# Optimization experiments

Measured on AMD Instinct MI355X. Metric: run time of the kernel, lower is better.

The kernel has to match this reference:

```python
import jax, jax.numpy as jnp
import numpy as np
import math

N_NODES = 50000
N_EDGES = 800000
HIDDEN = 128
NUM_GAUSS = 50
NUM_FILTERS = 128
CUTOFF = 10.0
SHIFT = math.log(2.0)


def setup_inputs() -> dict:
    key = jax.random.key(0)
    ks = jax.random.split(key, 12)
    x = jax.random.normal(ks[0], (N_NODES, HIDDEN), dtype=jnp.float32)
    edge_index = jax.random.randint(ks[1], (2, N_EDGES), 0, N_NODES, dtype=jnp.int64)
    edge_weight = jax.random.uniform(ks[2], (N_EDGES,), dtype=jnp.float32)
    edge_attr = jax.random.normal(ks[3], (N_EDGES, NUM_GAUSS), dtype=jnp.float32)
    # learned parameters (xavier-ish scale)
    def xavier(k, shape):
        fan_in, fan_out = shape[1], shape[0]
        bound = math.sqrt(6.0 / (fan_in + fan_out))
        return jax.random.uniform(k, shape, dtype=jnp.float32, minval=-bound, maxval=bound)
    mlp_w1 = xavier(ks[4], (NUM_FILTERS, NUM_GAUSS))
    mlp_b1 = jnp.zeros((NUM_FILTERS,), jnp.float32)
    mlp_w2 = xavier(ks[5], (NUM_FILTERS, NUM_FILTERS))
    mlp_b2 = jnp.zeros((NUM_FILTERS,), jnp.float32)
    lin1_w = xavier(ks[6], (NUM_FILTERS, HIDDEN))   # no bias
    lin2_w = xavier(ks[7], (HIDDEN, NUM_FILTERS))
    lin2_b = jnp.zeros((HIDDEN,), jnp.float32)
    lin_w = xavier(ks[8], (HIDDEN, HIDDEN))
    lin_b = jnp.zeros((HIDDEN,), jnp.float32)
    return {"x": x, "edge_index": edge_index, "edge_weight": edge_weight,
            "edge_attr": edge_attr, "mlp_w1": mlp_w1, "mlp_b1": mlp_b1,
            "mlp_w2": mlp_w2, "mlp_b2": mlp_b2, "lin1_w": lin1_w,
            "lin2_w": lin2_w, "lin2_b": lin2_b, "lin_w": lin_w, "lin_b": lin_b}


def shifted_softplus(v):
    return jax.nn.softplus(v) - SHIFT


def reference(x, edge_index, edge_weight, edge_attr, mlp_w1, mlp_b1,
              mlp_w2, mlp_b2, lin1_w, lin2_w, lin2_b, lin_w, lin_b):
    src, dst = edge_index[0], edge_index[1]
    # cosine cutoff per edge: [E]
    C = 0.5 * (jnp.cos(edge_weight * (jnp.pi / CUTOFF)) + 1.0)
    # edge filter MLP: [E, num_filters]
    h_e = shifted_softplus(edge_attr @ mlp_w1.T + mlp_b1)
    W = (h_e @ mlp_w2.T + mlp_b2) * C[:, None]
    # node projection, gather-multiply-scatter aggregation
    h = x @ lin1_w.T                       # [N, num_filters]
    msg = h[src] * W                       # [E, num_filters]
    agg = jax.ops.segment_sum(msg, dst, num_segments=N_NODES)  # [N, num_filters]
    h = agg @ lin2_w.T + lin2_b            # [N, hidden]
    h = shifted_softplus(h)
    out = h @ lin_w.T + lin_b              # [N, hidden]
    return out
```

## Files before the change

### kernel.cpp

```cpp
#include <hip/hip_runtime.h>
#include <hip/hip_bf16.h>
#include <math.h>

#define E_NUM 800000
#define NN 50000
#define NG 50
#define NTW (E_NUM / 16)
#define EDGE_BLOCKS 512

typedef __bf16 bf16x8 __attribute__((ext_vector_type(8)));
typedef float f32x4 __attribute__((ext_vector_type(4)));
typedef unsigned short ushortx8 __attribute__((ext_vector_type(8)));

__device__ __forceinline__ unsigned short f2b(float f) {
  union { __bf16 h; unsigned short u; } v; v.h = (__bf16)f; return v.u;
}
__device__ __forceinline__ float b2f(unsigned short u) {
  union { unsigned u; float f; } v; v.u = ((unsigned)u) << 16; return v.f;
}
__device__ __forceinline__ float sspf(float v) {
  float e = __builtin_amdgcn_exp2f(-1.4426950408889634f * fabsf(v));
  return fmaxf(v, 0.f) + 0.6931471805599453f * __builtin_amdgcn_logf(fmaf(0.5f, e, 0.5f));
}

__device__ __forceinline__ void gather_attr(const float* __restrict__ attr, int idx, int q,
                                            bf16x8& ua, bf16x8& ub) {
  const float* rp = attr + (long)idx * NG;
  float2 p0 = *(const float2*)(rp + q * 8);
  float2 p1 = *(const float2*)(rp + q * 8 + 2);
  float2 p2 = *(const float2*)(rp + q * 8 + 4);
  float2 p3 = *(const float2*)(rp + q * 8 + 6);
  float2 p4 = {0.f, 0.f}, p5 = {0.f, 0.f}, p6 = {0.f, 0.f}, p7 = {0.f, 0.f};
  if (q < 2) {
    const float* rp2 = rp + 32 + q * 8;
    p4 = *(const float2*)(rp2);
    p5 = *(const float2*)(rp2 + 2);
    p6 = *(const float2*)(rp2 + 4);
    p7 = *(const float2*)(rp2 + 6);
  } else if (q == 2) {
    p4 = *(const float2*)(rp + 48);
  }
  union { ushortx8 u; bf16x8 b; } a, bb;
  a.u[0] = f2b(p0.x); a.u[1] = f2b(p0.y); a.u[2] = f2b(p1.x); a.u[3] = f2b(p1.y);
  a.u[4] = f2b(p2.x); a.u[5] = f2b(p2.y); a.u[6] = f2b(p3.x); a.u[7] = f2b(p3.y);
  bb.u[0] = f2b(p4.x); bb.u[1] = f2b(p4.y); bb.u[2] = f2b(p5.x); bb.u[3] = f2b(p5.y);
  bb.u[4] = f2b(p6.x); bb.u[5] = f2b(p6.y); bb.u[6] = f2b(p7.x); bb.u[7] = f2b(p7.y);
  ua = a.b; ub = bb.b;
}

__global__ __launch_bounds__(256) void k_hist(const int* __restrict__ ei, int* __restrict__ counts) {
  int e = blockIdx.x * 256 + threadIdx.x;
  if (e < E_NUM) atomicAdd(&counts[ei[E_NUM + e]], 1);
}

__global__ __launch_bounds__(1024) void k_scan(const int* __restrict__ counts,
                                               int* __restrict__ cursor) {
  __shared__ int tot[1024];
  const int t = threadIdx.x;
  const int C = (NN + 1023) >> 10;
  int lo = t * C, hi = lo + C; if (hi > NN) hi = NN; if (lo > NN) lo = NN;
  int s = 0;
  for (int i = lo; i < hi; ++i) s += counts[i];
  tot[t] = s;
  __syncthreads();
  int mine = s;
  for (int o = 1; o < 1024; o <<= 1) {
    int v = (t >= o) ? tot[t - o] : 0;
    __syncthreads();
    tot[t] += v;
    __syncthreads();
  }
  int run = tot[t] - mine;
  for (int i = lo; i < hi; ++i) { int c = counts[i]; cursor[i] = run; run += c; }
}

__global__ __launch_bounds__(256) void k_scatter2(
    const int* __restrict__ ei, const float* __restrict__ ew,
    int* __restrict__ cursor, int* __restrict__ srcS, int* __restrict__ dstS,
    float* __restrict__ cS, int* __restrict__ eS)
{
  int e = blockIdx.x * 256 + threadIdx.x;
  if (e >= E_NUM) return;
  int d = ei[E_NUM + e];
  int pos = atomicAdd(&cursor[d], 1);
  srcS[pos] = ei[e];
  dstS[pos] = d;
  cS[pos] = 0.5f * (__builtin_amdgcn_cosf(ew[e] * 0.05f) + 1.f);
  eS[pos] = e;
}

__global__ __launch_bounds__(256) void k_mfma_gemm(
    const float* __restrict__ X, const float* __restrict__ Wm,
    const float* __restrict__ bias, float* __restrict__ out, int act, int nrows)
{
  __shared__ __attribute__((aligned(16))) unsigned short s_x[128 * 128];
  __shared__ __attribute__((aligned(16))) unsigned short s_w[128 * 128];
  const int tid = threadIdx.x;
  const int w = tid >> 6, lane = tid & 63, q = lane >> 4, n16 = lane & 15;
  const int base = blockIdx.x * 128;

  for (int c = tid; c < 128 * 16; c += 256) {
    int f = c >> 4, ch = c & 15;
    const float4* wp = (const float4*)(Wm + f * 128 + ch * 8);
    float4 v0 = wp[0], v1 = wp[1];
    ushortx8 v = { f2b(v0.x), f2b(v0.y), f2b(v0.z), f2b(v0.w),
                   f2b(v1.x), f2b(v1.y), f2b(v1.z), f2b(v1.w) };
    *(ushortx8*)&s_w[(f << 7) + ((ch ^ (f & 15)) << 3)] = v;
  }
  for (int c = tid; c < 128 * 16; c += 256) {
    int r = c >> 4, ch = c & 15;
    int n = base + r;
    float4 v0 = {0.f, 0.f, 0.f, 0.f}, v1 = v0;
    if (n < nrows) {
      const float4* xp = (const float4*)(X + (long)n * 128 + ch * 8);
      v0 = xp[0]; v1 = xp[1];
    }
    ushortx8 v = { f2b(v0.x), f2b(v0.y), f2b(v0.z), f2b(v0.w),
                   f2b(v1.x), f2b(v1.y), f2b(v1.z), f2b(v1.w) };
    *(ushortx8*)&s_x[(r << 7) + ((ch ^ (r & 15)) << 3)] = v;
  }
  __syncthreads();

  float bv[8];
#pragma unroll
  for (int t = 0; t < 8; ++t) bv[t] = bias ? bias[t * 16 + n16] : 0.f;

  bf16x8 a[2][4];
#pragma unroll
  for (int g = 0; g < 2; ++g) {
    int r = w * 32 + g * 16 + n16;
#pragma unroll
    for (int ks = 0; ks < 4; ++ks)
      a[g][ks] = *(const bf16x8*)&s_x[(r << 7) + (((ks * 4 + q) ^ (r & 15)) << 3)];
  }
#pragma unroll
  for (int t = 0; t < 8; ++t) {
    int f = t * 16 + n16;
    bf16x8 b[4];
#pragma unroll
    for (int ks = 0; ks < 4; ++ks)
      b[ks] = *(const bf16x8*)&s_w[(f << 7) + (((ks * 4 + q) ^ (f & 15)) << 3)];
#pragma unroll
    for (int g = 0; g < 2; ++g) {
      f32x4 acc = {0.f, 0.f, 0.f, 0.f};
#pragma unroll
      for (int ks = 0; ks < 4; ++ks)
        acc = __builtin_amdgcn_mfma_f32_16x16x32_bf16(a[g][ks], b[ks], acc, 0, 0, 0);
#pragma unroll
      for (int r = 0; r < 4; ++r) {
        int n = base + w * 32 + g * 16 + q * 4 + r;
        if (n < nrows) {
          float v = acc[r] + bv[t];
          if (act) v = sspf(v);
          out[(long)n * 128 + f] = v;
        }
      }
    }
  }
}

__global__ __launch_bounds__(256, 2) void k_gemm23(
    const float* __restrict__ A, const float* __restrict__ W2,
    const float* __restrict__ B2, const float* __restrict__ W3,
    const float* __restrict__ B3, float* __restrict__ out, int nrows)
{
  __shared__ __attribute__((aligned(16))) unsigned short s_x[128 * 128];
  __shared__ __attribute__((aligned(16))) unsigned short s_w[128 * 128];
  const int tid = threadIdx.x;
  const int w = tid >> 6, lane = tid & 63, q = lane >> 4, n16 = lane & 15;
  const int base = blockIdx.x * 128;

  for (int c = tid; c < 128 * 16; c += 256) {
    int f = c >> 4, ch = c & 15;
    const float4* wp = (const float4*)(W2 + f * 128 + ch * 8);
    float4 v0 = wp[0], v1 = wp[1];
    ushortx8 v = { f2b(v0.x), f2b(v0.y), f2b(v0.z), f2b(v0.w),
                   f2b(v1.x), f2b(v1.y), f2b(v1.z), f2b(v1.w) };
    *(ushortx8*)&s_w[(f << 7) + ((ch ^ (f & 15)) << 3)] = v;
  }
  for (int c = tid; c < 128 * 16; c += 256) {
    int r = c >> 4, ch = c & 15;
    int n = base + r;
    float4 v0 = {0.f, 0.f, 0.f, 0.f}, v1 = v0;
    if (n < nrows) {
      const float4* xp = (const float4*)(A + (long)n * 128 + ch * 8);
      v0 = xp[0]; v1 = xp[1];
    }
    ushortx8 v = { f2b(v0.x), f2b(v0.y), f2b(v0.z), f2b(v0.w),
                   f2b(v1.x), f2b(v1.y), f2b(v1.z), f2b(v1.w) };
    *(ushortx8*)&s_x[(r << 7) + ((ch ^ (r & 15)) << 3)] = v;
  }
  __syncthreads();

  float b2v[8], b3v[8];
#pragma unroll
  for (int t = 0; t < 8; ++t) { b2v[t] = B2[t * 16 + n16]; b3v[t] = B3[t * 16 + n16]; }

  bf16x8 a[2][4];
#pragma unroll
  for (int g = 0; g < 2; ++g) {
    int r = w * 32 + g * 16 + n16;
#pragma unroll
    for (int ks = 0; ks < 4; ++ks)
      a[g][ks] = *(const bf16x8*)&s_x[(r << 7) + (((ks * 4 + q) ^ (r & 15)) << 3)];
  }
  float acc1[8][2][4];
#pragma unroll
  for (int t = 0; t < 8; ++t) {
    int f = t * 16 + n16;
    bf16x8 b[4];
#pragma unroll
    for (int ks = 0; ks < 4; ++ks)
      b[ks] = *(const bf16x8*)&s_w[(f << 7) + (((ks * 4 + q) ^ (f & 15)) << 3)];
#pragma unroll
    for (int g = 0; g < 2; ++g) {
      f32x4 acc = {0.f, 0.f, 0.f, 0.f};
#pragma unroll
      for (int ks = 0; ks < 4; ++ks)
        acc = __builtin_amdgcn_mfma_f32_16x16x32_bf16(a[g][ks], b[ks], acc, 0, 0, 0);
#pragma unroll
      for (int r = 0; r < 4; ++r) acc1[t][g][r] = acc[r];
    }
  }
  __syncthreads();

#pragma unroll
  for (int t = 0; t < 8; ++t) {
    int f = t * 16 + n16;
#pragma unroll
    for (int g = 0; g < 2; ++g)
#pragma unroll
      for (int r = 0; r < 4; ++r) {
        int row = w * 32 + g * 16 + q * 4 + r;
        s_x[(row << 7) + (((f >> 3) ^ (row & 15)) << 3) + (f & 7)] =
            f2b(sspf(acc1[t][g][r] + b2v[t]));
      }
  }
  for (int c = tid; c < 128 * 16; c += 256) {
    int f = c >> 4, ch = c & 15;
    const float4* wp = (const float4*)(W3 + f * 128 + ch * 8);
    float4 v0 = wp[0], v1 = wp[1];
    ushortx8 v = { f2b(v0.x), f2b(v0.y), f2b(v0.z), f2b(v0.w),
                   f2b(v1.x), f2b(v1.y), f2b(v1.z), f2b(v1.w) };
    *(ushortx8*)&s_w[(f << 7) + ((ch ^ (f & 15)) << 3)] = v;
  }
  __syncthreads();

#pragma unroll
  for (int g = 0; g < 2; ++g) {
    int r = w * 32 + g * 16 + n16;
#pragma unroll
    for (int ks = 0; ks < 4; ++ks)
      a[g][ks] = *(const bf16x8*)&s_x[(r << 7) + (((ks * 4 + q) ^ (r & 15)) << 3)];
  }
#pragma unroll
  for (int t = 0; t < 8; ++t) {
    int f = t * 16 + n16;
    bf16x8 b[4];
#pragma unroll
    for (int ks = 0; ks < 4; ++ks)
      b[ks] = *(const bf16x8*)&s_w[(f << 7) + (((ks * 4 + q) ^ (f & 15)) << 3)];
#pragma unroll
    for (int g = 0; g < 2; ++g) {
      f32x4 acc = {0.f, 0.f, 0.f, 0.f};
#pragma unroll
      for (int ks = 0; ks < 4; ++ks)
        acc = __builtin_amdgcn_mfma_f32_16x16x32_bf16(a[g][ks], b[ks], acc, 0, 0, 0);
#pragma unroll
      for (int r = 0; r < 4; ++r) {
        int n = base + w * 32 + g * 16 + q * 4 + r;
        if (n < nrows) out[(long)n * 128 + f] = acc[r] + b3v[t];
      }
    }
  }
}

__global__ __launch_bounds__(512, 4) void k_edge_agg(
    const float* __restrict__ attr, const int* __restrict__ ei,
    const float* __restrict__ ew, const float* __restrict__ w1,
    const float* __restrict__ b1, const float* __restrict__ w2,
    const float* __restrict__ b2, const float* __restrict__ h,
    const int* __restrict__ srcS, const int* __restrict__ dstS,
    const float* __restrict__ cS, const int* __restrict__ eS,
    float* __restrict__ agg, int mode)
{
  __shared__ __attribute__((aligned(16))) unsigned short s_w2[128 * 128];
  __shared__ __attribute__((aligned(16))) unsigned short s_scr[8 * 16 * 136];

  const int tid  = threadIdx.x;
  const int w    = tid >> 6;
  const int lane = tid & 63;
  const int q    = lane >> 4;
  const int n16  = lane & 15;

  for (int i = tid; i < 128 * 128; i += 512) {
    int f = i >> 7, k = i & 127;
    int pos = (f << 7) + ((((k >> 3) ^ (f & 15)) << 3)) + (k & 7);
    s_w2[pos] = f2b(w2[i]);
  }
  bf16x8 w1A[8], w1B[8];
#pragma unroll
  for (int t = 0; t < 8; ++t) {
    int f = t * 16 + n16;
    const float* row = w1 + f * NG;
    union { ushortx8 u; bf16x8 b; } ua, ub;
#pragma unroll
    for (int j = 0; j < 8; ++j) ua.u[j] = f2b(row[q * 8 + j]);
#pragma unroll
    for (int j = 0; j < 8; ++j) { int k = 32 + q * 8 + j; ub.u[j] = (k < NG) ? f2b(row[k]) : (unsigned short)0; }
    w1A[t] = ua.b; w1B[t] = ub.b;
  }
  float b1v[8], b2v[8];
#pragma unroll
  for (int t = 0; t < 8; ++t) {
    b1v[t] = b1[t * 16 + n16];
    b2v[t] = b2[t * 16 + n16];
  }
  __syncthreads();

  unsigned short* scr = s_scr + w * (16 * 136);
  const int nwaves = EDGE_BLOCKS * 8;
  const int gw = blockIdx.x * 8 + w;

  if (mode == 1) {
    bf16x8 uaN = {}, ubN = {};
    int idxN = 0;
    if (gw < NTW) {
      int idx0 = eS[(long)gw * 16 + n16];
      gather_attr(attr, idx0, q, uaN, ubN);
      if (gw + nwaves < NTW) idxN = eS[(long)(gw + nwaves) * 16 + n16];
    }

    for (int tile = gw; tile < NTW; tile += nwaves) {
      const int e0 = tile * 16;
      const bf16x8 uaC = uaN, ubC = ubN;

#pragma unroll
      for (int t = 0; t < 8; ++t) {
        f32x4 acc = {0.f, 0.f, 0.f, 0.f};
        acc = __builtin_amdgcn_mfma_f32_16x16x32_bf16(uaC, w1A[t], acc, 0, 0, 0);
        acc = __builtin_amdgcn_mfma_f32_16x16x32_bf16(ubC, w1B[t], acc, 0, 0, 0);
        int f = t * 16 + n16;
#pragma unroll
        for (int r = 0; r < 4; ++r) {
          int row = q * 4 + r;
          scr[row * 136 + f] = f2b(sspf(acc[r] + b1v[t]));
        }
      }
      __builtin_amdgcn_wave_barrier();

      bf16x8 a2f[4];
#pragma unroll
      for (int ks = 0; ks < 4; ++ks)
        a2f[ks] = *(const bf16x8*)&scr[n16 * 136 + ks * 32 + q * 8];
      __builtin_amdgcn_wave_barrier();

      const int tn = tile + nwaves;
      if (tn < NTW) gather_attr(attr, idxN, q, uaN, ubN);
      if (tn + nwaves < NTW) idxN = eS[(long)(tn + nwaves) * 16 + n16];

      float cvv[4];
#pragma unroll
      for (int r = 0; r < 4; ++r) cvv[r] = cS[e0 + q * 4 + r];

#pragma unroll
      for (int t = 0; t < 8; ++t) {
        int f = t * 16 + n16;
        f32x4 acc = {0.f, 0.f, 0.f, 0.f};
#pragma unroll
        for (int ks = 0; ks < 4; ++ks) {
          bf16x8 bb = *(const bf16x8*)&s_w2[(f << 7) + (((ks * 4 + q) ^ (f & 15)) << 3)];
          acc = __builtin_amdgcn_mfma_f32_16x16x32_bf16(a2f[ks], bb, acc, 0, 0, 0);
        }
#pragma unroll
        for (int r = 0; r < 4; ++r) {
          int row = q * 4 + r;
          scr[row * 136 + f] = f2b((acc[r] + b2v[t]) * cvv[r]);
        }
      }
      __builtin_amdgcn_wave_barrier();

      int dcur = -1, rowstart = 0;
      float ax = 0.f, ay = 0.f;
#pragma unroll
      for (int hf = 0; hf < 2; ++hf) {
        int dv[8]; float2 hv[8];
#pragma unroll
        for (int i = 0; i < 8; ++i) {
          int pos = e0 + hf * 8 + i;
          dv[i] = __builtin_amdgcn_readfirstlane(dstS[pos]);
          int sv = __builtin_amdgcn_readfirstlane(srcS[pos]);
          hv[i] = *(const float2*)(h + (long)sv * 128 + (lane << 1));
        }
#pragma unroll
        for (int i = 0; i < 8; ++i) {
          int row = hf * 8 + i;
          if (dv[i] != dcur) {
            if (dcur >= 0) {
              float* ap = agg + (long)dcur * 128 + (lane << 1);
              if (rowstart == 0) { atomicAdd(ap, ax); atomicAdd(ap + 1, ay); }
              else { float2 o; o.x = ax; o.y = ay; *(float2*)ap = o; }
            }
            dcur = dv[i]; ax = 0.f; ay = 0.f; rowstart = row;
          }
          unsigned wp = *(const unsigned*)&scr[row * 136 + (lane << 1)];
          ax = fmaf(hv[i].x, b2f((unsigned short)(wp & 0xffffu)), ax);
          ay = fmaf(hv[i].y, b2f((unsigned short)(wp >> 16)), ay);
        }
      }
      {
        float* ap = agg + (long)dcur * 128 + (lane << 1);
        atomicAdd(ap, ax); atomicAdd(ap + 1, ay);
      }
      __builtin_amdgcn_wave_barrier();
    }
  } else {
    for (int tile = gw; tile < NTW; tile += nwaves) {
      const int e0 = tile * 16;
      bf16x8 ua, ub;
      gather_attr(attr, e0 + n16, q, ua, ub);

#pragma unroll
      for (int t = 0; t < 8; ++t) {
        f32x4 acc = {0.f, 0.f, 0.f, 0.f};
        acc = __builtin_amdgcn_mfma_f32_16x16x32_bf16(ua, w1A[t], acc, 0, 0, 0);
        acc = __builtin_amdgcn_mfma_f32_16x16x32_bf16(ub, w1B[t], acc, 0, 0, 0);
        int f = t * 16 + n16;
#pragma unroll
        for (int r = 0; r < 4; ++r) {
          int row = q * 4 + r;
          scr[row * 136 + f] = f2b(sspf(acc[r] + b1v[t]));
        }
      }
      __builtin_amdgcn_wave_barrier();

      bf16x8 a2f[4];
#pragma unroll
      for (int ks = 0; ks < 4; ++ks)
        a2f[ks] = *(const bf16x8*)&scr[n16 * 136 + ks * 32 + q * 8];
      __builtin_amdgcn_wave_barrier();

      float cvv[4];
      int srcv[4], dstv[4];
#pragma unroll
      for (int r = 0; r < 4; ++r) {
        cvv[r] = 0.5f * (__builtin_amdgcn_cosf(ew[e0 + q * 4 + r] * 0.05f) + 1.f);
        srcv[r] = ei[e0 + q * 4 + r];
        dstv[r] = ei[E_NUM + e0 + q * 4 + r];
      }

#pragma unroll
      for (int t = 0; t < 8; ++t) {
        int f = t * 16 + n16;
        f32x4 acc = {0.f, 0.f, 0.f, 0.f};
#pragma unroll
        for (int ks = 0; ks < 4; ++ks) {
          bf16x8 bb = *(const bf16x8*)&s_w2[(f << 7) + (((ks * 4 + q) ^ (f & 15)) << 3)];
          acc = __builtin_amdgcn_mfma_f32_16x16x32_bf16(a2f[ks], bb, acc, 0, 0, 0);
        }
#pragma unroll
        for (int r = 0; r < 4; ++r) {
          float msg = h[(long)srcv[r] * 128 + f] * (acc[r] + b2v[t]) * cvv[r];
          atomicAdd(&agg[(long)dstv[r] * 128 + f], msg);
        }
      }
      __builtin_amdgcn_wave_barrier();
    }
  }
}

extern "C" void kernel_launch(void* const* d_in, const int* in_sizes, int n_in,
                              void* d_out, int out_size, void* d_ws, size_t ws_size,
                              hipStream_t stream) {
  const float* x     = (const float*)d_in[0];
  const int*   ei    = (const int*)  d_in[1];
  const float* ew    = (const float*)d_in[2];
  const float* attr  = (const float*)d_in[3];
  const float* w1    = (const float*)d_in[4];
  const float* b1    = (const float*)d_in[5];
  const float* w2    = (const float*)d_in[6];
  const float* b2    = (const float*)d_in[7];
  const float* lin1w = (const float*)d_in[8];
  const float* lin2w = (const float*)d_in[9];
  const float* lin2b = (const float*)d_in[10];
  const float* linw  = (const float*)d_in[11];
  const float* linb  = (const float*)d_in[12];
  float* out = (float*)d_out;

  char* base = (char*)d_ws;
  float* agg    = (float*)base;
  float* h      = agg + (size_t)NN * 128;
  int*   counts = (int*)(h + (size_t)NN * 128);
  int*   cursor = counts + NN;
  int*   srcS   = cursor + NN;
  int*   dstS   = srcS + E_NUM;
  float* cS     = (float*)(dstS + E_NUM);
  int*   eS     = (int*)(cS + E_NUM);
  size_t need   = (size_t)((char*)(eS + E_NUM) - base);
  const int mode = (ws_size >= need) ? 1 : 0;

  const int gemm_grid = (NN + 127) / 128;
  (void)hipMemsetAsync(agg, 0, (size_t)NN * 128 * sizeof(float), stream);
  if (mode == 1) {
    (void)hipMemsetAsync(counts, 0, (size_t)NN * sizeof(int), stream);
    k_hist<<<(E_NUM + 255) / 256, 256, 0, stream>>>(ei, counts);
    k_scan<<<1, 1024, 0, stream>>>(counts, cursor);
    k_scatter2<<<(E_NUM + 255) / 256, 256, 0, stream>>>(ei, ew, cursor, srcS, dstS, cS, eS);
  }
  k_mfma_gemm<<<gemm_grid, 256, 0, stream>>>(x, lin1w, nullptr, h, 0, NN);
  k_edge_agg<<<EDGE_BLOCKS, 512, 0, stream>>>(attr, ei, ew, w1, b1, w2, b2, h,
                                              srcS, dstS, cS, eS, agg, mode);
  k_gemm23<<<gemm_grid, 256, 0, stream>>>(agg, lin2w, lin2b, linw, linb, out, NN);
}
```

Baseline: 618.9 us.

## Pre-convert weights to bf16 once and read them from global instead of LDS

A new kernel converts the four 128x128 weight matrices to bf16 once into the workspace. The node GEMMs and the edge kernel then read B operands straight from global/L2 instead of staging them in shared memory. This drops the per-block LDS weight load and __syncthreads, and shrinks LDS so more blocks fit per CU (launch bounds raised, 768 edge blocks, 64-row GEMM tiles). The edge MFMA loop is partially unrolled to ease register pressure. In exchange, every MFMA now depends on global-memory latency for its weight fragments and on L2 hit rates.

```diff
diff --git a/kernel.cpp b/kernel.cpp
--- a/kernel.cpp
+++ b/kernel.cpp
@@ -6,7 +6,7 @@
 #define NN 50000
 #define NG 50
 #define NTW (E_NUM / 16)
-#define EDGE_BLOCKS 512
+#define EDGE_BLOCKS 768
 
 typedef __bf16 bf16x8 __attribute__((ext_vector_type(8)));
 typedef float f32x4 __attribute__((ext_vector_type(4)));
@@ -48,6 +48,17 @@
   ua = a.b; ub = bb.b;
 }
 
+__global__ __launch_bounds__(256) void k_cvtw4(
+    const float* __restrict__ a0, const float* __restrict__ a1,
+    const float* __restrict__ a2, const float* __restrict__ a3,
+    unsigned short* __restrict__ o)
+{
+  int i = blockIdx.x * 256 + threadIdx.x;
+  int m = i >> 14, k = i & 16383;
+  const float* s = (m == 0) ? a0 : (m == 1) ? a1 : (m == 2) ? a2 : a3;
+  o[i] = f2b(s[k]);
+}
+
 __global__ __launch_bounds__(256) void k_hist(const int* __restrict__ ei, int* __restrict__ counts) {
   int e = blockIdx.x * 256 + threadIdx.x;
   if (e < E_NUM) atomicAdd(&counts[ei[E_NUM + e]], 1);
@@ -89,202 +100,117 @@
   eS[pos] = e;
 }
 
-__global__ __launch_bounds__(256) void k_mfma_gemm(
-    const float* __restrict__ X, const float* __restrict__ Wm,
-    const float* __restrict__ bias, float* __restrict__ out, int act, int nrows)
+__global__ __launch_bounds__(256, 4) void k_gemm1(
+    const float* __restrict__ X, const unsigned short* __restrict__ Wb,
+    float* __restrict__ out)
 {
-  __shared__ __attribute__((aligned(16))) unsigned short s_x[128 * 128];
-  __shared__ __attribute__((aligned(16))) unsigned short s_w[128 * 128];
-  const int tid = threadIdx.x;
-  const int w = tid >> 6, lane = tid & 63, q = lane >> 4, n16 = lane & 15;
-  const int base = blockIdx.x * 128;
-
-  for (int c = tid; c < 128 * 16; c += 256) {
-    int f = c >> 4, ch = c & 15;
-    const float4* wp = (const float4*)(Wm + f * 128 + ch * 8);
-    float4 v0 = wp[0], v1 = wp[1];
-    ushortx8 v = { f2b(v0.x), f2b(v0.y), f2b(v0.z), f2b(v0.w),
-                   f2b(v1.x), f2b(v1.y), f2b(v1.z), f2b(v1.w) };
-    *(ushortx8*)&s_w[(f << 7) + ((ch ^ (f & 15)) << 3)] = v;
-  }
-  for (int c = tid; c < 128 * 16; c += 256) {
-    int r = c >> 4, ch = c & 15;
-    int n = base + r;
+  const int w = threadIdx.x >> 6, lane = threadIdx.x & 63;
+  const int q = lane >> 4, n16 = lane & 15;
+  const int rb = blockIdx.x * 64 + w * 16;
+  const int r = rb + n16;
+
+  bf16x8 a[4];
+#pragma unroll
+  for (int ks = 0; ks < 4; ++ks) {
     float4 v0 = {0.f, 0.f, 0.f, 0.f}, v1 = v0;
-    if (n < nrows) {
-      const float4* xp = (const float4*)(X + (long)n * 128 + ch * 8);
+    if (r < NN) {
+      const float4* xp = (const float4*)(X + (long)r * 128 + ks * 32 + q * 8);
       v0 = xp[0]; v1 = xp[1];
     }
-    ushortx8 v = { f2b(v0.x), f2b(v0.y), f2b(v0.z), f2b(v0.w),
-                   f2b(v1.x), f2b(v1.y), f2b(v1.z), f2b(v1.w) };
-    *(ushortx8*)&s_x[(r << 7) + ((ch ^ (r & 15)) << 3)] = v;
-  }
-  __syncthreads();
-
-  float bv[8];
-#pragma unroll
-  for (int t = 0; t < 8; ++t) bv[t] = bias ? bias[t * 16 + n16] : 0.f;
-
-  bf16x8 a[2][4];
-#pragma unroll
-  for (int g = 0; g < 2; ++g) {
-    int r = w * 32 + g * 16 + n16;
-#pragma unroll
-    for (int ks = 0; ks < 4; ++ks)
-      a[g][ks] = *(const bf16x8*)&s_x[(r << 7) + (((ks * 4 + q) ^ (r & 15)) << 3)];
-  }
-#pragma unroll
-  for (int t = 0; t < 8; ++t) {
-    int f = t * 16 + n16;
-    bf16x8 b[4];
-#pragma unroll
-    for (int ks = 0; ks < 4; ++ks)
-      b[ks] = *(const bf16x8*)&s_w[(f << 7) + (((ks * 4 + q) ^ (f & 15)) << 3)];
-#pragma unroll
-    for (int g = 0; g < 2; ++g) {
-      f32x4 acc = {0.f, 0.f, 0.f, 0.f};
-#pragma unroll
-      for (int ks = 0; ks < 4; ++ks)
-        acc = __builtin_amdgcn_mfma_f32_16x16x32_bf16(a[g][ks], b[ks], acc, 0, 0, 0);
-#pragma unroll
-      for (int r = 0; r < 4; ++r) {
-        int n = base + w * 32 + g * 16 + q * 4 + r;
-        if (n < nrows) {
-          float v = acc[r] + bv[t];
-          if (act) v = sspf(v);
-          out[(long)n * 128 + f] = v;
-        }
-      }
-    }
-  }
-}
-
-__global__ __launch_bounds__(256, 2) void k_gemm23(
-    const float* __restrict__ A, const float* __restrict__ W2,
-    const float* __restrict__ B2, const float* __restrict__ W3,
-    const float* __restrict__ B3, float* __restrict__ out, int nrows)
+    union { ushortx8 u; bf16x8 b; } t;
+    t.u[0] = f2b(v0.x); t.u[1] = f2b(v0.y); t.u[2] = f2b(v0.z); t.u[3] = f2b(v0.w);
+    t.u[4] = f2b(v1.x); t.u[5] = f2b(v1.y); t.u[6] = f2b(v1.z); t.u[7] = f2b(v1.w);
+    a[ks] = t.b;
+  }
+#pragma unroll
+  for (int t8 = 0; t8 < 8; ++t8) {
+    int f = t8 * 16 + n16;
+    f32x4 acc = {0.f, 0.f, 0.f, 0.f};
+#pragma unroll
+    for (int ks = 0; ks < 4; ++ks) {
+      bf16x8 b = *(const bf16x8*)(Wb + (f << 7) + ks * 32 + q * 8);
+      acc = __builtin_amdgcn_mfma_f32_16x16x32_bf16(a[ks], b, acc, 0, 0, 0);
+    }
+#pragma unroll
+    for (int ri = 0; ri < 4; ++ri) {
+      int n = rb + q * 4 + ri;
+      if (n < NN) out[(long)n * 128 + f] = acc[ri];
+    }
+  }
+}
+
+__global__ __launch_bounds__(256, 4) void k_gemm23(
+    const float* __restrict__ A, const unsigned short* __restrict__ W2b,
+    const float* __restrict__ B2, const unsigned short* __restrict__ W3b,
+    const float* __restrict__ B3, float* __restrict__ out)
 {
-  __shared__ __attribute__((aligned(16))) unsigned short s_x[128 * 128];
-  __shared__ __attribute__((aligned(16))) unsigned short s_w[128 * 128];
-  const int tid = threadIdx.x;
-  const int w = tid >> 6, lane = tid & 63, q = lane >> 4, n16 = lane & 15;
-  const int base = blockIdx.x * 128;
-
-  for (int c = tid; c < 128 * 16; c += 256) {
-    int f = c >> 4, ch = c & 15;
-    const float4* wp = (const float4*)(W2 + f * 128 + ch * 8);
-    float4 v0 = wp[0], v1 = wp[1];
-    ushortx8 v = { f2b(v0.x), f2b(v0.y), f2b(v0.z), f2b(v0.w),
-                   f2b(v1.x), f2b(v1.y), f2b(v1.z), f2b(v1.w) };
-    *(ushortx8*)&s_w[(f << 7) + ((ch ^ (f & 15)) << 3)] = v;
-  }
-  for (int c = tid; c < 128 * 16; c += 256) {
-    int r = c >> 4, ch = c & 15;
-    int n = base + r;
+  __shared__ __attribute__((aligned(16))) unsigned short s_scr[4 * 16 * 136];
+  const int w = threadIdx.x >> 6, lane = threadIdx.x & 63;
+  const int q = lane >> 4, n16 = lane & 15;
+  const int rb = blockIdx.x * 64 + w * 16;
+  const int r = rb + n16;
+  unsigned short* scr = s_scr + w * (16 * 136);
+
+  bf16x8 a[4];
+#pragma unroll
+  for (int ks = 0; ks < 4; ++ks) {
     float4 v0 = {0.f, 0.f, 0.f, 0.f}, v1 = v0;
-    if (n < nrows) {
-      const float4* xp = (const float4*)(A + (long)n * 128 + ch * 8);
+    if (r < NN) {
+      const float4* xp = (const float4*)(A + (long)r * 128 + ks * 32 + q * 8);
       v0 = xp[0]; v1 = xp[1];
     }
-    ushortx8 v = { f2b(v0.x), f2b(v0.y), f2b(v0.z), f2b(v0.w),
-                   f2b(v1.x), f2b(v1.y), f2b(v1.z), f2b(v1.w) };
-    *(ushortx8*)&s_x[(r << 7) + ((ch ^ (r & 15)) << 3)] = v;
-  }
-  __syncthreads();
-
-  float b2v[8], b3v[8];
-#pragma unroll
-  for (int t = 0; t < 8; ++t) { b2v[t] = B2[t * 16 + n16]; b3v[t] = B3[t * 16 + n16]; }
-
-  bf16x8 a[2][4];
-#pragma unroll
-  for (int g = 0; g < 2; ++g) {
-    int r = w * 32 + g * 16 + n16;
-#pragma unroll
-    for (int ks = 0; ks < 4; ++ks)
-      a[g][ks] = *(const bf16x8*)&s_x[(r << 7) + (((ks * 4 + q) ^ (r & 15)) << 3)];
-  }
-  float acc1[8][2][4];
-#pragma unroll
-  for (int t = 0; t < 8; ++t) {
-    int f = t * 16 + n16;
-    bf16x8 b[4];
-#pragma unroll
-    for (int ks = 0; ks < 4; ++ks)
-      b[ks] = *(const bf16x8*)&s_w[(f << 7) + (((ks * 4 + q) ^ (f & 15)) << 3)];
-#pragma unroll
-    for (int g = 0; g < 2; ++g) {
-      f32x4 acc = {0.f, 0.f, 0.f, 0.f};
-#pragma unroll
-      for (int ks = 0; ks < 4; ++ks)
-        acc = __builtin_amdgcn_mfma_f32_16x16x32_bf16(a[g][ks], b[ks], acc, 0, 0, 0);
-#pragma unroll
-      for (int r = 0; r < 4; ++r) acc1[t][g][r] = acc[r];
-    }
-  }
-  __syncthreads();
-
-#pragma unroll
-  for (int t = 0; t < 8; ++t) {
-    int f = t * 16 + n16;
-#pragma unroll
-    for (int g = 0; g < 2; ++g)
-#pragma unroll
-      for (int r = 0; r < 4; ++r) {
-        int row = w * 32 + g * 16 + q * 4 + r;
-        s_x[(row << 7) + (((f >> 3) ^ (row & 15)) << 3) + (f & 7)] =
-            f2b(sspf(acc1[t][g][r] + b2v[t]));
-      }
-  }
-  for (int c = tid; c < 128 * 16; c += 256) {
-    int f = c >> 4, ch = c & 15;
-    const float4* wp = (const float4*)(W3 + f * 128 + ch * 8);
-    float4 v0 = wp[0], v1 = wp[1];
-    ushortx8 v = { f2b(v0.x), f2b(v0.y), f2b(v0.z), f2b(v0.w),
-                   f2b(v1.x), f2b(v1.y), f2b(v1.z), f2b(v1.w) };
-    *(ushortx8*)&s_w[(f << 7) + ((ch ^ (f & 15)) << 3)] = v;
-  }
-  __syncthreads();
-
-#pragma unroll
-  for (int g = 0; g < 2; ++g) {
-    int r = w * 32 + g * 16 + n16;
-#pragma unroll
-    for (int ks = 0; ks < 4; ++ks)
-      a[g][ks] = *(const bf16x8*)&s_x[(r << 7) + (((ks * 4 + q) ^ (r & 15)) << 3)];
-  }
-#pragma unroll
-  for (int t = 0; t < 8; ++t) {
-    int f = t * 16 + n16;
-    bf16x8 b[4];
-#pragma unroll
-    for (int ks = 0; ks < 4; ++ks)
-      b[ks] = *(const bf16x8*)&s_w[(f << 7) + (((ks * 4 + q) ^ (f & 15)) << 3)];
-#pragma unroll
-    for (int g = 0; g < 2; ++g) {
-      f32x4 acc = {0.f, 0.f, 0.f, 0.f};
-#pragma unroll
-      for (int ks = 0; ks < 4; ++ks)
-        acc = __builtin_amdgcn_mfma_f32_16x16x32_bf16(a[g][ks], b[ks], acc, 0, 0, 0);
-#pragma unroll
-      for (int r = 0; r < 4; ++r) {
-        int n = base + w * 32 + g * 16 + q * 4 + r;
-        if (n < nrows) out[(long)n * 128 + f] = acc[r] + b3v[t];
-      }
-    }
-  }
-}
-
-__global__ __launch_bounds__(512, 4) void k_edge_agg(
+    union { ushortx8 u; bf16x8 b; } t;
+    t.u[0] = f2b(v0.x); t.u[1] = f2b(v0.y); t.u[2] = f2b(v0.z); t.u[3] = f2b(v0.w);
+    t.u[4] = f2b(v1.x); t.u[5] = f2b(v1.y); t.u[6] = f2b(v1.z); t.u[7] = f2b(v1.w);
+    a[ks] = t.b;
+  }
+#pragma unroll
+  for (int t8 = 0; t8 < 8; ++t8) {
+    int f = t8 * 16 + n16;
+    f32x4 acc = {0.f, 0.f, 0.f, 0.f};
+#pragma unroll
+    for (int ks = 0; ks < 4; ++ks) {
+      bf16x8 b = *(const bf16x8*)(W2b + (f << 7) + ks * 32 + q * 8);
+      acc = __builtin_amdgcn_mfma_f32_16x16x32_bf16(a[ks], b, acc, 0, 0, 0);
+    }
+    float bias = B2[f];
+#pragma unroll
+    for (int ri = 0; ri < 4; ++ri)
+      scr[(q * 4 + ri) * 136 + f] = f2b(sspf(acc[ri] + bias));
+  }
+  __builtin_amdgcn_wave_barrier();
+  bf16x8 a2[4];
+#pragma unroll
+  for (int ks = 0; ks < 4; ++ks)
+    a2[ks] = *(const bf16x8*)&scr[n16 * 136 + ks * 32 + q * 8];
+  __builtin_amdgcn_wave_barrier();
+#pragma unroll
+  for (int t8 = 0; t8 < 8; ++t8) {
+    int f = t8 * 16 + n16;
+    f32x4 acc = {0.f, 0.f, 0.f, 0.f};
+#pragma unroll
+    for (int ks = 0; ks < 4; ++ks) {
+      bf16x8 b = *(const bf16x8*)(W3b + (f << 7) + ks * 32 + q * 8);
+      acc = __builtin_amdgcn_mfma_f32_16x16x32_bf16(a2[ks], b, acc, 0, 0, 0);
+    }
+    float bias = B3[f];
+#pragma unroll
+    for (int ri = 0; ri < 4; ++ri) {
+      int n = rb + q * 4 + ri;
+      if (n < NN) out[(long)n * 128 + f] = acc[ri] + bias;
+    }
+  }
+}
+
+__global__ __launch_bounds__(512, 6) void k_edge_agg(
     const float* __restrict__ attr, const int* __restrict__ ei,
     const float* __restrict__ ew, const float* __restrict__ w1,
-    const float* __restrict__ b1, const float* __restrict__ w2,
+    const float* __restrict__ b1, const unsigned short* __restrict__ w2b,
     const float* __restrict__ b2, const float* __restrict__ h,
     const int* __restrict__ srcS, const int* __restrict__ dstS,
     const float* __restrict__ cS, const int* __restrict__ eS,
     float* __restrict__ agg, int mode)
 {
-  __shared__ __attribute__((aligned(16))) unsigned short s_w2[128 * 128];
   __shared__ __attribute__((aligned(16))) unsigned short s_scr[8 * 16 * 136];
 
   const int tid  = threadIdx.x;
@@ -293,11 +219,6 @@
   const int q    = lane >> 4;
   const int n16  = lane & 15;
 
-  for (int i = tid; i < 128 * 128; i += 512) {
-    int f = i >> 7, k = i & 127;
-    int pos = (f << 7) + ((((k >> 3) ^ (f & 15)) << 3)) + (k & 7);
-    s_w2[pos] = f2b(w2[i]);
-  }
   bf16x8 w1A[8], w1B[8];
 #pragma unroll
   for (int t = 0; t < 8; ++t) {
@@ -316,7 +237,6 @@
     b1v[t] = b1[t * 16 + n16];
     b2v[t] = b2[t * 16 + n16];
   }
-  __syncthreads();
 
   unsigned short* scr = s_scr + w * (16 * 136);
   const int nwaves = EDGE_BLOCKS * 8;
@@ -363,13 +283,13 @@
 #pragma unroll
       for (int r = 0; r < 4; ++r) cvv[r] = cS[e0 + q * 4 + r];
 
-#pragma unroll
+#pragma unroll 2
       for (int t = 0; t < 8; ++t) {
         int f = t * 16 + n16;
         f32x4 acc = {0.f, 0.f, 0.f, 0.f};
 #pragma unroll
         for (int ks = 0; ks < 4; ++ks) {
-          bf16x8 bb = *(const bf16x8*)&s_w2[(f << 7) + (((ks * 4 + q) ^ (f & 15)) << 3)];
+          bf16x8 bb = *(const bf16x8*)(w2b + (f << 7) + ks * 32 + q * 8);
           acc = __builtin_amdgcn_mfma_f32_16x16x32_bf16(a2f[ks], bb, acc, 0, 0, 0);
         }
 #pragma unroll
@@ -449,13 +369,13 @@
         dstv[r] = ei[E_NUM + e0 + q * 4 + r];
       }
 
-#pragma unroll
+#pragma unroll 2
       for (int t = 0; t < 8; ++t) {
         int f = t * 16 + n16;
         f32x4 acc = {0.f, 0.f, 0.f, 0.f};
 #pragma unroll
         for (int ks = 0; ks < 4; ++ks) {
-          bf16x8 bb = *(const bf16x8*)&s_w2[(f << 7) + (((ks * 4 + q) ^ (f & 15)) << 3)];
+          bf16x8 bb = *(const bf16x8*)(w2b + (f << 7) + ks * 32 + q * 8);
           acc = __builtin_amdgcn_mfma_f32_16x16x32_bf16(a2f[ks], bb, acc, 0, 0, 0);
         }
 #pragma unroll
@@ -492,23 +412,31 @@
   float* h      = agg + (size_t)NN * 128;
   int*   counts = (int*)(h + (size_t)NN * 128);
   int*   cursor = counts + NN;
-  int*   srcS   = cursor + NN;
+  size_t whead  = (size_t)((char*)(cursor + NN) - base);
+  size_t woff   = (whead + 255) & ~(size_t)255;
+  unsigned short* wb = (unsigned short*)(base + woff);
+  unsigned short* w2b    = wb;
+  unsigned short* lin1wb = wb + 16384;
+  unsigned short* lin2wb = wb + 32768;
+  unsigned short* linwb  = wb + 49152;
+  int*   srcS   = (int*)(wb + 65536);
   int*   dstS   = srcS + E_NUM;
   float* cS     = (float*)(dstS + E_NUM);
   int*   eS     = (int*)(cS + E_NUM);
   size_t need   = (size_t)((char*)(eS + E_NUM) - base);
   const int mode = (ws_size >= need) ? 1 : 0;
 
-  const int gemm_grid = (NN + 127) / 128;
   (void)hipMemsetAsync(agg, 0, (size_t)NN * 128 * sizeof(float), stream);
+  k_cvtw4<<<256, 256, 0, stream>>>(w2, lin1w, lin2w, linw, wb);
   if (mode == 1) {
     (void)hipMemsetAsync(counts, 0, (size_t)NN * sizeof(int), stream);
     k_hist<<<(E_NUM + 255) / 256, 256, 0, stream>>>(ei, counts);
     k_scan<<<1, 1024, 0, stream>>>(counts, cursor);
     k_scatter2<<<(E_NUM + 255) / 256, 256, 0, stream>>>(ei, ew, cursor, srcS, dstS, cS, eS);
   }
-  k_mfma_gemm<<<gemm_grid, 256, 0, stream>>>(x, lin1w, nullptr, h, 0, NN);
-  k_edge_agg<<<EDGE_BLOCKS, 512, 0, stream>>>(attr, ei, ew, w1, b1, w2, b2, h,
+  const int ggrid = (NN + 63) / 64;
+  k_gemm1<<<ggrid, 256, 0, stream>>>(x, lin1wb, h);
+  k_edge_agg<<<EDGE_BLOCKS, 512, 0, stream>>>(attr, ei, ew, w1, b1, w2b, b2, h,
                                               srcS, dstS, cS, eS, agg, mode);
-  k_gemm23<<<gemm_grid, 256, 0, stream>>>(agg, lin2w, lin2b, linw, linb, out, NN);
-}
+  k_gemm23<<<ggrid, 256, 0, stream>>>(agg, lin2wb, lin2b, linwb, linb, out);
+}
```

Measured after the change: 858.3 us. 1.39x slower.
